# Performance work log

Hardware: AMD Instinct MI355X
Metric: run time of the kernel (lower is better)

Reference implementation:

```python
import jax, jax.numpy as jnp
import numpy as np

ANCHORS = np.array([[1.4940052559648322, 2.3598481287086823],
                    [4.0113013115312155, 5.760873975661669]], dtype=np.float32)
THRESH = 0.6
OBJ_SCALE = 5.0
NOOBJ_SCALE = 1.0


def setup_inputs() -> dict:
    key = jax.random.key(0)
    k1, k2, k3 = jax.random.split(key, 3)
    nB, nA, nH, nW = 128, 2, 128, 128
    output = jax.random.normal(k1, (nB, nA * 5, nH, nW), dtype=jnp.float32)
    xy = jax.random.uniform(k2, (nB, 2), jnp.float32, 0.1, 0.9)   # box centers, normalized
    wh = jax.random.uniform(k3, (nB, 2), jnp.float32, 0.05, 0.4)  # box sizes, normalized
    target = jnp.concatenate([xy, wh], axis=1)  # [nB, 4] = (x, y, w, h)
    anchors = jnp.asarray(ANCHORS)
    return {"output": output, "target": target, "anchors": anchors}


def reference(output, target, anchors):
    nB, _, nH, nW = output.shape
    nA = anchors.shape[0]
    # [nB, nA, nH, nW, 5]
    out = output.reshape(nB, nA, 5, nH, nW).transpose(0, 1, 3, 4, 2)
    x = jax.nn.sigmoid(out[..., 0])
    y = jax.nn.sigmoid(out[..., 1])
    w = out[..., 2]
    h = out[..., 3]
    conf = jax.nn.sigmoid(out[..., 4])

    # torch code uses .data / Variable() everywhere in target construction -> no grads flow there
    tgt = jax.lax.stop_gradient(target)
    anc = jax.lax.stop_gradient(anchors)
    sg = jax.lax.stop_gradient

    fW = jnp.asarray(nW, dtype=x.dtype)
    fH = jnp.asarray(nH, dtype=x.dtype)
    grid_x = jnp.arange(nW, dtype=x.dtype)[None, None, None, :]
    grid_y = jnp.arange(nH, dtype=x.dtype)[None, None, :, None]
    aw = anc[:, 0][None, :, None, None]
    ah = anc[:, 1][None, :, None, None]

    # detached predicted boxes in grid units (cx, cy, w, h)
    pb_x = sg(x) + grid_x
    pb_y = sg(y) + grid_y
    pb_w = jnp.exp(sg(w)) * aw
    pb_h = jnp.exp(sg(h)) * ah

    gt_x = tgt[:, 0] * fW
    gt_y = tgt[:, 1] * fH
    gt_w = tgt[:, 2] * fW
    gt_h = tgt[:, 3] * fH
    gx4 = gt_x[:, None, None, None]
    gy4 = gt_y[:, None, None, None]
    gw4 = gt_w[:, None, None, None]
    gh4 = gt_h[:, None, None, None]

    # vectorized bbox_iou (x1y1x2y2=False), faithful to the scalar torch loop
    mx = jnp.minimum(pb_x - pb_w * 0.5, gx4 - gw4 * 0.5)
    Mx = jnp.maximum(pb_x + pb_w * 0.5, gx4 + gw4 * 0.5)
    my = jnp.minimum(pb_y - pb_h * 0.5, gy4 - gh4 * 0.5)
    My = jnp.maximum(pb_y + pb_h * 0.5, gy4 + gh4 * 0.5)
    uw = Mx - mx
    uh = My - my
    cw = pb_w + gw4 - uw
    ch = pb_h + gh4 - uh
    carea = cw * ch
    uarea = pb_w * pb_h + gw4 * gh4 - carea
    iou = jnp.where((cw <= 0) | (ch <= 0), jnp.zeros((), x.dtype), carea / uarea)

    noobj_mask = iou <= THRESH  # [nB, nA, nH, nW]

    # best anchor per GT via wh-IoU (bbox_anchor_iou)
    inter = jnp.minimum(gt_w[:, None], anc[None, :, 0]) * jnp.minimum(gt_h[:, None], anc[None, :, 1])
    union = gt_w[:, None] * gt_h[:, None] + 1e-16 + anc[None, :, 0] * anc[None, :, 1] - inter
    best_n = jnp.argmax(inter / union, axis=1)  # [nB]

    gxi = gt_x.astype(jnp.int32)
    gyi = gt_y.astype(jnp.int32)
    b_idx = jnp.arange(nB)
    noobj_mask = noobj_mask.at[b_idx, best_n, gyi, gxi].set(False)

    tx = gt_x - jnp.floor(gt_x)
    ty = gt_y - jnp.floor(gt_y)
    tw = jnp.log(gt_w / anc[best_n, 0] + 1e-16)
    th = jnp.log(gt_h / anc[best_n, 1] + 1e-16)
    scale = 2.0 - tgt[:, 2] * tgt[:, 3]  # [nB]

    x_s = x[b_idx, best_n, gyi, gxi]
    y_s = y[b_idx, best_n, gyi, gxi]
    w_s = w[b_idx, best_n, gyi, gxi]
    h_s = h[b_idx, best_n, gyi, gxi]
    conf_s = conf[b_idx, best_n, gyi, gxi]

    loss_x = jnp.mean((x_s * scale - tx * scale) ** 2)
    loss_y = jnp.mean((y_s * scale - ty * scale) ** 2)
    loss_w = jnp.mean((w_s * scale - tw * scale) ** 2)
    loss_h = jnp.mean((h_s * scale - th * scale) ** 2)

    n_noobj = jnp.sum(noobj_mask).astype(conf.dtype)
    loss_conf = (OBJ_SCALE * jnp.mean((conf_s - 1.0) ** 2)
                 + NOOBJ_SCALE * jnp.sum(jnp.where(noobj_mask, conf * conf, 0.0)) / n_noobj)

    return loss_x + loss_y + loss_w + loss_h + loss_conf
```

## Files before the change

kernel.cpp:

```cpp
#include <hip/hip_runtime.h>

#define NB 128
#define NA 2
#define NH 128
#define NW 128
#define PLANE (NH * NW)
#define RTHRESH 0.6f
#define OBJ_SCALE 5.0f
#define NBLK 4096

__device__ __forceinline__ float sigm(float v) {
    return 1.0f / (1.0f + __expf(-v));
}

__device__ __forceinline__ void batch_const(const float* __restrict__ target,
                                            const float* __restrict__ anchors,
                                            int b,
                                            float& gx, float& gy, float& gw, float& gh,
                                            int& bn, int& gxi, int& gyi) {
    float t0 = target[b * 4 + 0], t1 = target[b * 4 + 1];
    float t2 = target[b * 4 + 2], t3 = target[b * 4 + 3];
    gx = t0 * (float)NW;
    gy = t1 * (float)NH;
    gw = t2 * (float)NW;
    gh = t3 * (float)NH;
    float a0w = anchors[0], a0h = anchors[1];
    float a1w = anchors[2], a1h = anchors[3];
    float i0 = fminf(gw, a0w) * fminf(gh, a0h);
    float u0 = gw * gh + 1e-16f + a0w * a0h - i0;
    float i1 = fminf(gw, a1w) * fminf(gh, a1h);
    float u1 = gw * gh + 1e-16f + a1w * a1h - i1;
    bn  = (i1 / u1 > i0 / u0) ? 1 : 0;
    gxi = (int)gx;
    gyi = (int)gy;
}

__global__ __launch_bounds__(256) void region_main(
        const float* __restrict__ out,
        const float* __restrict__ target,
        const float* __restrict__ anchors,
        float* __restrict__ psum,
        unsigned int* __restrict__ pcnt) {
    int tid = threadIdx.x;
    int idx4 = blockIdx.x * 256 + tid;
    int j0 = (idx4 & 31) * 4;
    int i  = (idx4 >> 5) & 127;
    int a  = (idx4 >> 12) & 1;
    int b  = idx4 >> 13;

    float gx, gy, gw, gh; int bn, gxi, gyi;
    batch_const(target, anchors, b, gx, gy, gw, gh, bn, gxi, gyi);
    float aw = anchors[a * 2 + 0];
    float ah = anchors[a * 2 + 1];

    size_t base = (size_t)(b * 10 + a * 5) * PLANE + (size_t)i * NW + (size_t)j0;
    float4 vx = *(const float4*)(out + base);
    float4 vy = *(const float4*)(out + base + 1 * PLANE);
    float4 vw = *(const float4*)(out + base + 2 * PLANE);
    float4 vh = *(const float4*)(out + base + 3 * PLANE);
    float4 vc = *(const float4*)(out + base + 4 * PLANE);

    float gxm = gx - gw * 0.5f, gxM = gx + gw * 0.5f;
    float gym = gy - gh * 0.5f, gyM = gy + gh * 0.5f;
    float garea = gw * gh;
    bool row_sel = (a == bn) && (i == gyi);

    float lsum = 0.0f;
    int   lcnt = 0;

    const float* fx = (const float*)&vx;
    const float* fy = (const float*)&vy;
    const float* fw = (const float*)&vw;
    const float* fh = (const float*)&vh;
    const float* fc = (const float*)&vc;

#pragma unroll
    for (int e = 0; e < 4; ++e) {
        float px = sigm(fx[e]) + (float)(j0 + e);
        float py = sigm(fy[e]) + (float)i;
        float pw = __expf(fw[e]) * aw;
        float ph = __expf(fh[e]) * ah;
        float cf = sigm(fc[e]);

        float mx = fminf(px - pw * 0.5f, gxm);
        float Mx = fmaxf(px + pw * 0.5f, gxM);
        float my = fminf(py - ph * 0.5f, gym);
        float My = fmaxf(py + ph * 0.5f, gyM);
        float cw = pw + gw - (Mx - mx);
        float ch = ph + gh - (My - my);
        float iou = 0.0f;
        if (cw > 0.0f && ch > 0.0f) {
            float carea = cw * ch;
            iou = carea / (pw * ph + garea - carea);
        }
        bool noobj = (iou <= RTHRESH) && !(row_sel && (j0 + e) == gxi);
        if (noobj) { lsum += cf * cf; lcnt += 1; }
    }

#pragma unroll
    for (int off = 32; off > 0; off >>= 1) {
        lsum += __shfl_down(lsum, off);
        lcnt += __shfl_down(lcnt, off);
    }
    __shared__ float ssum[4];
    __shared__ int   scnt[4];
    int wid = tid >> 6, lane = tid & 63;
    if (lane == 0) { ssum[wid] = lsum; scnt[wid] = lcnt; }
    __syncthreads();
    if (tid == 0) {
        psum[blockIdx.x] = ssum[0] + ssum[1] + ssum[2] + ssum[3];
        pcnt[blockIdx.x] = (unsigned int)(scnt[0] + scnt[1] + scnt[2] + scnt[3]);
    }
}

__global__ __launch_bounds__(1024) void region_final(
        const float* __restrict__ out,
        const float* __restrict__ target,
        const float* __restrict__ anchors,
        const float* __restrict__ psum,
        const unsigned int* __restrict__ pcnt,
        float* __restrict__ loss_out) {
    int t = threadIdx.x;
    float s = 0.0f;
    unsigned int c = 0;
#pragma unroll
    for (int k = 0; k < NBLK / 1024; ++k) {
        s += psum[t + k * 1024];
        c += pcnt[t + k * 1024];
    }

    float v = 0.0f;
    if (t < NB) {
        int b = t;
        float gx, gy, gw, gh; int bn, gxi, gyi;
        batch_const(target, anchors, b, gx, gy, gw, gh, bn, gxi, gyi);
        float tx = gx - floorf(gx);
        float ty = gy - floorf(gy);
        float aw = anchors[bn * 2 + 0];
        float ah = anchors[bn * 2 + 1];
        float tw = __logf(gw / aw + 1e-16f);
        float th = __logf(gh / ah + 1e-16f);
        float scale = 2.0f - target[b * 4 + 2] * target[b * 4 + 3];

        size_t base = (size_t)(b * 10 + bn * 5) * PLANE + (size_t)gyi * NW + (size_t)gxi;
        float xs = sigm(out[base]);
        float ys = sigm(out[base + 1 * PLANE]);
        float wr = out[base + 2 * PLANE];
        float hr = out[base + 3 * PLANE];
        float cs = sigm(out[base + 4 * PLANE]);

        float dx = (xs - tx) * scale;
        float dy = (ys - ty) * scale;
        float dw = (wr - tw) * scale;
        float dh = (hr - th) * scale;
        float dc = cs - 1.0f;
        v = dx * dx + dy * dy + dw * dw + dh * dh + OBJ_SCALE * dc * dc;
    }

#pragma unroll
    for (int off = 32; off > 0; off >>= 1) {
        s += __shfl_down(s, off);
        c += __shfl_down(c, off);
        v += __shfl_down(v, off);
    }
    __shared__ float ss[16];
    __shared__ unsigned int sc[16];
    __shared__ float sv[16];
    int wid = t >> 6, lane = t & 63;
    if (lane == 0) { ss[wid] = s; sc[wid] = c; sv[wid] = v; }
    __syncthreads();
    if (t < 16) {
        s = ss[t]; c = sc[t]; v = sv[t];
#pragma unroll
        for (int off = 8; off > 0; off >>= 1) {
            s += __shfl_down(s, off);
            c += __shfl_down(c, off);
            v += __shfl_down(v, off);
        }
        if (t == 0)
            loss_out[0] = v * (1.0f / (float)NB) + s / (float)c;
    }
}

extern "C" void kernel_launch(void* const* d_in, const int* in_sizes, int n_in,
                              void* d_out, int out_size, void* d_ws, size_t ws_size,
                              hipStream_t stream) {
    const float* output  = (const float*)d_in[0];
    const float* target  = (const float*)d_in[1];
    const float* anchors = (const float*)d_in[2];
    float* loss = (float*)d_out;

    float* psum = (float*)d_ws;
    unsigned int* pcnt = (unsigned int*)((char*)d_ws + NBLK * sizeof(float));

    region_main<<<NBLK, 256, 0, stream>>>(output, target, anchors, psum, pcnt);
    region_final<<<1, 1024, 0, stream>>>(output, target, anchors, psum, pcnt, loss);
}
```

Measured before the change: 121.6 us.

## Fuse main and final reduction into one cooperative persistent kernel

Replaces the two-kernel launch with a single cooperative launch of 1024 blocks that each loop over four sweeps of the data. A grid-wide sync follows, after which block 0 performs the final reduction and the per-batch object loss. This is meant to remove the second kernel launch and its gap, and to cut the number of partial sums. In exchange it adds grid-sync overhead and lowers parallelism per sweep. If the cooperative launch fails, the code falls back to two kernels.

```diff
diff --git a/kernel.cpp b/kernel.cpp
--- a/kernel.cpp
+++ b/kernel.cpp
@@ -1,4 +1,7 @@
 #include <hip/hip_runtime.h>
+#include <hip/hip_cooperative_groups.h>
+
+namespace cg = cooperative_groups;
 
 #define NB 128
 #define NA 2
@@ -7,7 +10,12 @@
 #define PLANE (NH * NW)
 #define RTHRESH 0.6f
 #define OBJ_SCALE 5.0f
-#define NBLK 4096
+
+#define GRID  1024
+#define TPB   256
+#define SWEEP (GRID * TPB)
+#define GRAN  (NB * NA * NH * NW / 4)
+#define KSW   (GRAN / SWEEP)
 
 __device__ __forceinline__ float sigm(float v) {
     return 1.0f / (1.0f + __expf(-v));
@@ -35,66 +43,134 @@
     gyi = (int)gy;
 }
 
-__global__ __launch_bounds__(256) void region_main(
+__device__ __forceinline__ void finale(const float* __restrict__ out,
+                                       const float* __restrict__ target,
+                                       const float* __restrict__ anchors,
+                                       const float* __restrict__ psum,
+                                       const unsigned int* __restrict__ pcnt,
+                                       float* __restrict__ loss_out,
+                                       int tid) {
+    float v = 0.0f;
+    if (tid < NB) {
+        int b = tid;
+        float gx, gy, gw, gh; int bn, gxi, gyi;
+        batch_const(target, anchors, b, gx, gy, gw, gh, bn, gxi, gyi);
+        size_t base = (size_t)(b * 10 + bn * 5) * PLANE + (size_t)gyi * NW + (size_t)gxi;
+        float xs = out[base];
+        float ys = out[base + 1 * PLANE];
+        float wr = out[base + 2 * PLANE];
+        float hr = out[base + 3 * PLANE];
+        float cs = out[base + 4 * PLANE];
+        float tx = gx - floorf(gx);
+        float ty = gy - floorf(gy);
+        float aw = anchors[bn * 2 + 0];
+        float ah = anchors[bn * 2 + 1];
+        float tw = __logf(gw / aw + 1e-16f);
+        float th = __logf(gh / ah + 1e-16f);
+        float scale = 2.0f - target[b * 4 + 2] * target[b * 4 + 3];
+        float dx = (sigm(xs) - tx) * scale;
+        float dy = (sigm(ys) - ty) * scale;
+        float dw = (wr - tw) * scale;
+        float dh = (hr - th) * scale;
+        float dc = sigm(cs) - 1.0f;
+        v = dx * dx + dy * dy + dw * dw + dh * dh + OBJ_SCALE * dc * dc;
+    }
+
+    float s = 0.0f;
+    unsigned int c = 0;
+#pragma unroll
+    for (int k = 0; k < GRID / TPB; ++k) {
+        s += psum[tid + k * TPB];
+        c += pcnt[tid + k * TPB];
+    }
+
+#pragma unroll
+    for (int off = 32; off > 0; off >>= 1) {
+        s += __shfl_down(s, off);
+        c += __shfl_down(c, off);
+        v += __shfl_down(v, off);
+    }
+    __shared__ float        fs[4];
+    __shared__ unsigned int fc[4];
+    __shared__ float        fv[4];
+    int wid = tid >> 6, lane = tid & 63;
+    if (lane == 0) { fs[wid] = s; fc[wid] = c; fv[wid] = v; }
+    __syncthreads();
+    if (tid == 0) {
+        float ssum = fs[0] + fs[1] + fs[2] + fs[3];
+        float csum = (float)(fc[0] + fc[1] + fc[2] + fc[3]);
+        float vsum = fv[0] + fv[1] + fv[2] + fv[3];
+        loss_out[0] = vsum * (1.0f / (float)NB) + ssum / csum;
+    }
+}
+
+__global__ __launch_bounds__(TPB, 4) void region_fused(
         const float* __restrict__ out,
         const float* __restrict__ target,
         const float* __restrict__ anchors,
         float* __restrict__ psum,
-        unsigned int* __restrict__ pcnt) {
+        unsigned int* __restrict__ pcnt,
+        float* __restrict__ loss_out,
+        int fused) {
     int tid = threadIdx.x;
-    int idx4 = blockIdx.x * 256 + tid;
-    int j0 = (idx4 & 31) * 4;
-    int i  = (idx4 >> 5) & 127;
-    int a  = (idx4 >> 12) & 1;
-    int b  = idx4 >> 13;
-
-    float gx, gy, gw, gh; int bn, gxi, gyi;
-    batch_const(target, anchors, b, gx, gy, gw, gh, bn, gxi, gyi);
-    float aw = anchors[a * 2 + 0];
-    float ah = anchors[a * 2 + 1];
-
-    size_t base = (size_t)(b * 10 + a * 5) * PLANE + (size_t)i * NW + (size_t)j0;
-    float4 vx = *(const float4*)(out + base);
-    float4 vy = *(const float4*)(out + base + 1 * PLANE);
-    float4 vw = *(const float4*)(out + base + 2 * PLANE);
-    float4 vh = *(const float4*)(out + base + 3 * PLANE);
-    float4 vc = *(const float4*)(out + base + 4 * PLANE);
-
-    float gxm = gx - gw * 0.5f, gxM = gx + gw * 0.5f;
-    float gym = gy - gh * 0.5f, gyM = gy + gh * 0.5f;
-    float garea = gw * gh;
-    bool row_sel = (a == bn) && (i == gyi);
+    int tg  = blockIdx.x * TPB + tid;
 
     float lsum = 0.0f;
     int   lcnt = 0;
 
-    const float* fx = (const float*)&vx;
-    const float* fy = (const float*)&vy;
-    const float* fw = (const float*)&vw;
-    const float* fh = (const float*)&vh;
-    const float* fc = (const float*)&vc;
-
-#pragma unroll
-    for (int e = 0; e < 4; ++e) {
-        float px = sigm(fx[e]) + (float)(j0 + e);
-        float py = sigm(fy[e]) + (float)i;
-        float pw = __expf(fw[e]) * aw;
-        float ph = __expf(fh[e]) * ah;
-        float cf = sigm(fc[e]);
-
-        float mx = fminf(px - pw * 0.5f, gxm);
-        float Mx = fmaxf(px + pw * 0.5f, gxM);
-        float my = fminf(py - ph * 0.5f, gym);
-        float My = fmaxf(py + ph * 0.5f, gyM);
-        float cw = pw + gw - (Mx - mx);
-        float ch = ph + gh - (My - my);
-        float iou = 0.0f;
-        if (cw > 0.0f && ch > 0.0f) {
-            float carea = cw * ch;
-            iou = carea / (pw * ph + garea - carea);
+#pragma unroll
+    for (int k = 0; k < KSW; ++k) {
+        int g  = tg + k * SWEEP;
+        int j0 = (g & 31) * 4;
+        int i  = (g >> 5) & 127;
+        int a  = (g >> 12) & 1;
+        int b  = g >> 13;
+
+        float gx, gy, gw, gh; int bn, gxi, gyi;
+        batch_const(target, anchors, b, gx, gy, gw, gh, bn, gxi, gyi);
+        float aw = anchors[a * 2 + 0];
+        float ah = anchors[a * 2 + 1];
+
+        size_t base = (size_t)(b * 10 + a * 5) * PLANE + (size_t)i * NW + (size_t)j0;
+        float4 vx = *(const float4*)(out + base);
+        float4 vy = *(const float4*)(out + base + 1 * PLANE);
+        float4 vw = *(const float4*)(out + base + 2 * PLANE);
+        float4 vh = *(const float4*)(out + base + 3 * PLANE);
+        float4 vc = *(const float4*)(out + base + 4 * PLANE);
+
+        float gxm = gx - gw * 0.5f, gxM = gx + gw * 0.5f;
+        float gym = gy - gh * 0.5f, gyM = gy + gh * 0.5f;
+        float garea = gw * gh;
+        bool row_sel = (a == bn) && (i == gyi);
+
+        const float* fx = (const float*)&vx;
+        const float* fy = (const float*)&vy;
+        const float* fw = (const float*)&vw;
+        const float* fh = (const float*)&vh;
+        const float* fc = (const float*)&vc;
+
+#pragma unroll
+        for (int e = 0; e < 4; ++e) {
+            float px = sigm(fx[e]) + (float)(j0 + e);
+            float py = sigm(fy[e]) + (float)i;
+            float pw = __expf(fw[e]) * aw;
+            float ph = __expf(fh[e]) * ah;
+            float cf = sigm(fc[e]);
+
+            float mx = fminf(px - pw * 0.5f, gxm);
+            float Mx = fmaxf(px + pw * 0.5f, gxM);
+            float my = fminf(py - ph * 0.5f, gym);
+            float My = fmaxf(py + ph * 0.5f, gyM);
+            float cw = pw + gw - (Mx - mx);
+            float ch = ph + gh - (My - my);
+            float iou = 0.0f;
+            if (cw > 0.0f && ch > 0.0f) {
+                float carea = cw * ch;
+                iou = carea / (pw * ph + garea - carea);
+            }
+            bool noobj = (iou <= RTHRESH) && !(row_sel && (j0 + e) == gxi);
+            if (noobj) { lsum += cf * cf; lcnt += 1; }
         }
-        bool noobj = (iou <= RTHRESH) && !(row_sel && (j0 + e) == gxi);
-        if (noobj) { lsum += cf * cf; lcnt += 1; }
     }
 
 #pragma unroll
@@ -111,88 +187,49 @@
         psum[blockIdx.x] = ssum[0] + ssum[1] + ssum[2] + ssum[3];
         pcnt[blockIdx.x] = (unsigned int)(scnt[0] + scnt[1] + scnt[2] + scnt[3]);
     }
-}
-
-__global__ __launch_bounds__(1024) void region_final(
+
+    if (!fused) return;
+
+    __threadfence();
+    cg::this_grid().sync();
+
+    if (blockIdx.x != 0) return;
+    finale(out, target, anchors, psum, pcnt, loss_out, tid);
+}
+
+__global__ __launch_bounds__(TPB) void region_final2(
         const float* __restrict__ out,
         const float* __restrict__ target,
         const float* __restrict__ anchors,
         const float* __restrict__ psum,
         const unsigned int* __restrict__ pcnt,
         float* __restrict__ loss_out) {
-    int t = threadIdx.x;
-    float s = 0.0f;
-    unsigned int c = 0;
-#pragma unroll
-    for (int k = 0; k < NBLK / 1024; ++k) {
-        s += psum[t + k * 1024];
-        c += pcnt[t + k * 1024];
-    }
-
-    float v = 0.0f;
-    if (t < NB) {
-        int b = t;
-        float gx, gy, gw, gh; int bn, gxi, gyi;
-        batch_const(target, anchors, b, gx, gy, gw, gh, bn, gxi, gyi);
-        float tx = gx - floorf(gx);
-        float ty = gy - floorf(gy);
-        float aw = anchors[bn * 2 + 0];
-        float ah = anchors[bn * 2 + 1];
-        float tw = __logf(gw / aw + 1e-16f);
-        float th = __logf(gh / ah + 1e-16f);
-        float scale = 2.0f - target[b * 4 + 2] * target[b * 4 + 3];
-
-        size_t base = (size_t)(b * 10 + bn * 5) * PLANE + (size_t)gyi * NW + (size_t)gxi;
-        float xs = sigm(out[base]);
-        float ys = sigm(out[base + 1 * PLANE]);
-        float wr = out[base + 2 * PLANE];
-        float hr = out[base + 3 * PLANE];
-        float cs = sigm(out[base + 4 * PLANE]);
-
-        float dx = (xs - tx) * scale;
-        float dy = (ys - ty) * scale;
-        float dw = (wr - tw) * scale;
-        float dh = (hr - th) * scale;
-        float dc = cs - 1.0f;
-        v = dx * dx + dy * dy + dw * dw + dh * dh + OBJ_SCALE * dc * dc;
-    }
-
-#pragma unroll
-    for (int off = 32; off > 0; off >>= 1) {
-        s += __shfl_down(s, off);
-        c += __shfl_down(c, off);
-        v += __shfl_down(v, off);
-    }
-    __shared__ float ss[16];
-    __shared__ unsigned int sc[16];
-    __shared__ float sv[16];
-    int wid = t >> 6, lane = t & 63;
-    if (lane == 0) { ss[wid] = s; sc[wid] = c; sv[wid] = v; }
-    __syncthreads();
-    if (t < 16) {
-        s = ss[t]; c = sc[t]; v = sv[t];
-#pragma unroll
-        for (int off = 8; off > 0; off >>= 1) {
-            s += __shfl_down(s, off);
-            c += __shfl_down(c, off);
-            v += __shfl_down(v, off);
-        }
-        if (t == 0)
-            loss_out[0] = v * (1.0f / (float)NB) + s / (float)c;
-    }
+    finale(out, target, anchors, psum, pcnt, loss_out, threadIdx.x);
 }
 
 extern "C" void kernel_launch(void* const* d_in, const int* in_sizes, int n_in,
                               void* d_out, int out_size, void* d_ws, size_t ws_size,
                               hipStream_t stream) {
+    (void)in_sizes; (void)n_in; (void)out_size; (void)ws_size;
     const float* output  = (const float*)d_in[0];
     const float* target  = (const float*)d_in[1];
     const float* anchors = (const float*)d_in[2];
     float* loss = (float*)d_out;
 
     float* psum = (float*)d_ws;
-    unsigned int* pcnt = (unsigned int*)((char*)d_ws + NBLK * sizeof(float));
-
-    region_main<<<NBLK, 256, 0, stream>>>(output, target, anchors, psum, pcnt);
-    region_final<<<1, 1024, 0, stream>>>(output, target, anchors, psum, pcnt, loss);
-}
+    unsigned int* pcnt = (unsigned int*)((char*)d_ws + GRID * sizeof(float));
+
+    int fused = 1;
+    void* args[] = {(void*)&output, (void*)&target, (void*)&anchors,
+                    (void*)&psum, (void*)&pcnt, (void*)&loss, (void*)&fused};
+    hipError_t err = hipLaunchCooperativeKernel((const void*)region_fused,
+                                                dim3(GRID), dim3(TPB),
+                                                args, 0, stream);
+    if (err != hipSuccess) {
+        (void)hipGetLastError();
+        hipLaunchKernelGGL(region_fused, dim3(GRID), dim3(TPB), 0, stream,
+                           output, target, anchors, psum, pcnt, loss, 0);
+        hipLaunchKernelGGL(region_final2, dim3(1), dim3(TPB), 0, stream,
+                           output, target, anchors, psum, pcnt, loss);
+    }
+}
```

Result: slower. 302.4 us (+148.7%).
